# Kernel optimization log

Measured on AMD Instinct MI355X. Metric: run time of the kernel, lower is better.

## Reference

```python
import jax, jax.numpy as jnp
import numpy as np

PAD = float(-2**32 + 1)
NUM_HEADS = 16
LN_EPS = 1e-5


def _split_heads(x, h):
    # torch.cat(torch.chunk(x, h, dim=2), dim=0): head-major stacking
    B, T, D = x.shape
    d = D // h
    return x.reshape(B, T, h, d).transpose(2, 0, 1, 3).reshape(h * B, T, d)


def _merge_heads(x, h):
    # torch.cat(torch.chunk(x, h, dim=0), dim=2)
    hB, T, d = x.shape
    B = hB // h
    return x.reshape(h, B, T, d).transpose(1, 2, 0, 3).reshape(B, T, h * d)


def setup_inputs() -> dict:
    key = jax.random.key(0)
    ks = jax.random.split(key, 12)
    B, T, D = 2, 2048, 1024
    s = 1.0 / np.sqrt(D)
    return {
        "q": jax.random.normal(ks[0], (B, T, D), jnp.float32),
        "k": jax.random.normal(ks[1], (B, T, D), jnp.float32),
        "v": jax.random.normal(ks[2], (B, T, D), jnp.float32),
        "mask": jax.random.randint(ks[3], (B, T), 0, 2, jnp.int32),
        "causality": 0,
        "edge_fea": jnp.zeros((1,), jnp.float32),
        "wq": jax.random.normal(ks[4], (D, D), jnp.float32) * s,
        "bq": jax.random.normal(ks[5], (D,), jnp.float32) * 0.01,
        "wk": jax.random.normal(ks[6], (D, D), jnp.float32) * s,
        "bk": jax.random.normal(ks[7], (D,), jnp.float32) * 0.01,
        "wv": jax.random.normal(ks[8], (D, D), jnp.float32) * s,
        "bv": jax.random.normal(ks[9], (D,), jnp.float32) * 0.01,
        "gamma": jnp.ones((D,), jnp.float32),
        "beta": jnp.zeros((D,), jnp.float32),
    }


def reference(q, k, v, mask, causality, edge_fea, wq, bq, wk, bk, wv, bv, gamma, beta):
    h = NUM_HEADS
    B, T, D = q.shape
    depth = D // h

    qh = _split_heads(q @ wq.T + bq, h)   # (h*B, T, depth)
    kh = _split_heads(k @ wk.T + bk, h)
    vh = _split_heads(v @ wv.T + bv, h)

    scores = jnp.einsum('ntd,nsd->nts', qh, kh) / jnp.sqrt(jnp.asarray(depth, qh.dtype))
    # key mask: repeat_interleave over dim 0 (batch-major), 1 => masked
    km = jnp.repeat(mask.astype(scores.dtype), h, axis=0)[:, None, :]  # (h*B,1,T)
    scores = scores + km * PAD
    if causality:
        tril = jnp.tril(jnp.ones((T, T), scores.dtype))
        scores = jnp.where(tril[None] == 0, jnp.full_like(scores, PAD), scores)
    attn = jax.nn.softmax(scores, axis=-1)
    ctx = jnp.einsum('nts,nsd->ntd', attn, vh)

    out = _merge_heads(ctx, h) + q  # dropout is identity in eval mode
    # LayerNorm over last dim
    mu = jnp.mean(out, axis=-1, keepdims=True)
    var = jnp.var(out, axis=-1, keepdims=True)
    out = (out - mu) / jnp.sqrt(var + LN_EPS) * gamma + beta
    return out
```

## Files before the change

### kernel.cpp

```cpp
#include <hip/hip_runtime.h>
#include <hip/hip_bf16.h>
#include <stdint.h>

#define B_ 2
#define T_ 2048
#define D_ 1024
#define H_ 16
#define DEPTH 64
#define PADV (-4294967295.0f)

typedef unsigned short u16;
typedef unsigned int u32;
typedef short bf16x8 __attribute__((ext_vector_type(8)));
typedef float f32x4 __attribute__((ext_vector_type(4)));

#define MFMA16(a, b, c) __builtin_amdgcn_mfma_f32_16x16x32_bf16(a, b, c, 0, 0, 0)

#define GLOAD_LDS(g, l)                                                      \
    __builtin_amdgcn_global_load_lds(                                        \
        (__attribute__((address_space(1))) void*)(g),                        \
        (__attribute__((address_space(3))) void*)(l), 16, 0, 0)

__device__ __forceinline__ u16 f2bf(float f) {
    union { float f; u32 i; } x; x.f = f;
    u32 r = x.i + 0x7fffu + ((x.i >> 16) & 1u);
    return (u16)(r >> 16);
}
__device__ __forceinline__ uint2 pk4(float4 f) {
    return make_uint2((u32)f2bf(f.x) | ((u32)f2bf(f.y) << 16),
                      (u32)f2bf(f.z) | ((u32)f2bf(f.w) << 16));
}

__global__ __launch_bounds__(256) void conv_kernel(
    const float* __restrict__ s0, const float* __restrict__ s1, const float* __restrict__ s2,
    const float* __restrict__ s3, const float* __restrict__ s4, const float* __restrict__ s5,
    u16* __restrict__ xbf, u16* __restrict__ wbf)
{
    const int z = blockIdx.y;
    const float* src = (z == 0) ? s0 : (z == 1) ? s1 : (z == 2) ? s2
                     : (z == 3) ? s3 : (z == 4) ? s4 : s5;
    u16* dst = (z < 3) ? (xbf + (size_t)z * 4194304) : (wbf + (size_t)(z - 3) * 1048576);
    const size_t nel = (z < 3) ? 4194304u : 1048576u;
    for (size_t i = ((size_t)blockIdx.x * 256 + threadIdx.x) * 8; i < nel;
         i += (size_t)gridDim.x * 2048) {
        float4 a = *(const float4*)(src + i);
        float4 b = *(const float4*)(src + i + 4);
        uint2 lo = pk4(a), hi = pk4(b);
        *(uint4*)(dst + i) = make_uint4(lo.x, lo.y, hi.x, hi.y);
    }
}

__global__ __launch_bounds__(256, 3) void proj_mfma(
    const u16* __restrict__ xbf, const u16* __restrict__ wbf,
    const float* __restrict__ bq, const float* __restrict__ bk, const float* __restrict__ bv,
    u16* __restrict__ qh, u16* __restrict__ kh, u16* __restrict__ vt)
{
    __shared__ __attribute__((aligned(16))) u16 As[128 * 64];
    __shared__ __attribute__((aligned(16))) u16 Bs[128 * 64];

    const int z = blockIdx.z;
    const u16* A = xbf + (size_t)z * 4194304;
    const u16* W = wbf + (size_t)z * 1048576;
    const float* bias = (z == 0) ? bq : (z == 1) ? bk : bv;

    const int tid = threadIdx.x, w = tid >> 6, lane = tid & 63;
    const int quad = lane >> 4, l16 = lane & 15;
    const int m0 = blockIdx.y * 128, n0 = blockIdx.x * 128;
    const int wm = (w & 1) * 64, wn = (w >> 1) * 64;
    const int srow = lane >> 3;
    const int schunk = (lane & 7) ^ srow;

    f32x4 acc[4][4];
    #pragma unroll
    for (int mi = 0; mi < 4; ++mi)
        #pragma unroll
        for (int ni = 0; ni < 4; ++ni) acc[mi][ni] = (f32x4){0.f, 0.f, 0.f, 0.f};

    const size_t ar = (size_t)(m0 + 32 * w + srow);
    const size_t br = (size_t)(n0 + 32 * w + srow);

    for (int k0 = 0; k0 < D_; k0 += 64) {
        __syncthreads();
        #pragma unroll
        for (int i = 0; i < 4; ++i) {
            GLOAD_LDS(A + (ar + 8 * i) * D_ + k0 + schunk * 8, &As[(32 * w + 8 * i) * 64]);
            GLOAD_LDS(W + (br + 8 * i) * D_ + k0 + schunk * 8, &Bs[(32 * w + 8 * i) * 64]);
        }
        __syncthreads();

        #pragma unroll
        for (int kg = 0; kg < 2; ++kg) {
            const int ch = ((4 * kg + quad) ^ (l16 & 7)) * 8;
            bf16x8 af[4], bf[4];
            #pragma unroll
            for (int mi = 0; mi < 4; ++mi)
                af[mi] = *(const bf16x8*)&As[(wm + 16 * mi + l16) * 64 + ch];
            #pragma unroll
            for (int ni = 0; ni < 4; ++ni)
                bf[ni] = *(const bf16x8*)&Bs[(wn + 16 * ni + l16) * 64 + ch];
            #pragma unroll
            for (int mi = 0; mi < 4; ++mi)
                #pragma unroll
                for (int ni = 0; ni < 4; ++ni)
                    acc[mi][ni] = MFMA16(af[mi], bf[ni], acc[mi][ni]);
        }
    }

    float bl[4];
    #pragma unroll
    for (int ni = 0; ni < 4; ++ni) bl[ni] = bias[n0 + wn + ni * 16 + l16];

    #pragma unroll
    for (int mi = 0; mi < 4; ++mi) {
        const int mb = m0 + wm + mi * 16 + quad * 4;
        #pragma unroll
        for (int ni = 0; ni < 4; ++ni) {
            const int nn = n0 + wn + ni * 16 + l16;
            const int head = nn >> 6, d = nn & 63;
            if (z < 2) {
                u16* outp = (z == 0) ? qh : kh;
                #pragma unroll
                for (int r = 0; r < 4; ++r) {
                    const int m = mb + r;
                    const int b = m >> 11, t = m & (T_ - 1);
                    outp[((size_t)(head * B_ + b) * T_ + t) * DEPTH + d] =
                        f2bf(acc[mi][ni][r] + bl[ni]);
                }
            } else {
                const int b = mb >> 11, t = mb & (T_ - 1);
                float4 f = make_float4(acc[mi][ni][0] + bl[ni], acc[mi][ni][1] + bl[ni],
                                       acc[mi][ni][2] + bl[ni], acc[mi][ni][3] + bl[ni]);
                *(uint2*)(vt + ((size_t)(head * B_ + b) * DEPTH + d) * T_ + t) = pk4(f);
            }
        }
    }
}

__global__ __launch_bounds__(256, 3) void proj_kernel(
    const float* __restrict__ qin, const float* __restrict__ kin, const float* __restrict__ vin,
    const float* __restrict__ wq, const float* __restrict__ bq,
    const float* __restrict__ wk, const float* __restrict__ bk,
    const float* __restrict__ wv, const float* __restrict__ bv,
    u16* __restrict__ qh, u16* __restrict__ kh, u16* __restrict__ vt)
{
    __shared__ __attribute__((aligned(16))) u16 As[128][56];
    __shared__ __attribute__((aligned(16))) u16 Bs[128][56];
    const int z = blockIdx.z;
    const float* A    = (z == 0) ? qin : (z == 1) ? kin : vin;
    const float* W    = (z == 0) ? wq  : (z == 1) ? wk  : wv;
    const float* bias = (z == 0) ? bq  : (z == 1) ? bk  : bv;
    const int tid = threadIdx.x, w = tid >> 6, lane = tid & 63;
    const int quad = lane >> 4, l16 = lane & 15;
    const int m0 = blockIdx.y * 128, n0 = blockIdx.x * 128;
    const int wm = (w & 1) * 64, wn = (w >> 1) * 64;
    const int sr = tid >> 3, sc = (tid & 7) << 2;

    f32x4 acc[4][4];
    #pragma unroll
    for (int mi = 0; mi < 4; ++mi)
        #pragma unroll
        for (int ni = 0; ni < 4; ++ni) acc[mi][ni] = (f32x4){0.f, 0.f, 0.f, 0.f};

    for (int k0 = 0; k0 < D_; k0 += 32) {
        float4 av[4], wv4[4];
        #pragma unroll
        for (int g = 0; g < 4; ++g) {
            av[g]  = *(const float4*)(A + (size_t)(m0 + sr + g * 32) * D_ + k0 + sc);
            wv4[g] = *(const float4*)(W + (size_t)(n0 + sr + g * 32) * D_ + k0 + sc);
        }
        __syncthreads();
        #pragma unroll
        for (int g = 0; g < 4; ++g) {
            *(uint2*)&As[sr + g * 32][sc] = pk4(av[g]);
            *(uint2*)&Bs[sr + g * 32][sc] = pk4(wv4[g]);
        }
        __syncthreads();
        bf16x8 af[4], bf[4];
        #pragma unroll
        for (int mi = 0; mi < 4; ++mi)
            af[mi] = *(const bf16x8*)&As[wm + mi * 16 + l16][quad * 8];
        #pragma unroll
        for (int ni = 0; ni < 4; ++ni)
            bf[ni] = *(const bf16x8*)&Bs[wn + ni * 16 + l16][quad * 8];
        #pragma unroll
        for (int mi = 0; mi < 4; ++mi)
            #pragma unroll
            for (int ni = 0; ni < 4; ++ni)
                acc[mi][ni] = MFMA16(af[mi], bf[ni], acc[mi][ni]);
        __syncthreads();
    }
    float bl[4];
    #pragma unroll
    for (int ni = 0; ni < 4; ++ni) bl[ni] = bias[n0 + wn + ni * 16 + l16];
    #pragma unroll
    for (int mi = 0; mi < 4; ++mi) {
        const int mb = m0 + wm + mi * 16 + quad * 4;
        #pragma unroll
        for (int ni = 0; ni < 4; ++ni) {
            const int nn = n0 + wn + ni * 16 + l16;
            const int head = nn >> 6, d = nn & 63;
            if (z < 2) {
                u16* outp = (z == 0) ? qh : kh;
                #pragma unroll
                for (int r = 0; r < 4; ++r) {
                    const int m = mb + r;
                    const int b = m >> 11, t = m & (T_ - 1);
                    outp[((size_t)(head * B_ + b) * T_ + t) * DEPTH + d] =
                        f2bf(acc[mi][ni][r] + bl[ni]);
                }
            } else {
                const int b = mb >> 11, t = mb & (T_ - 1);
                float4 f = make_float4(acc[mi][ni][0] + bl[ni], acc[mi][ni][1] + bl[ni],
                                       acc[mi][ni][2] + bl[ni], acc[mi][ni][3] + bl[ni]);
                *(uint2*)(vt + ((size_t)(head * B_ + b) * DEPTH + d) * T_ + t) = pk4(f);
            }
        }
    }
}

__global__ __launch_bounds__(256, 4) void attn_kernel(
    const u16* __restrict__ qh, const u16* __restrict__ kh, const u16* __restrict__ vt,
    const int* __restrict__ maskp, const int* __restrict__ causp,
    float* __restrict__ outp)
{
    __shared__ __attribute__((aligned(16))) u16 Ks[64][72];
    __shared__ __attribute__((aligned(16))) u16 Vs[64][72];
    __shared__ __attribute__((aligned(16))) u16 Ps[4][16][72];

    const int n  = blockIdx.y;
    const int qt = blockIdx.x;
    const int head = n >> 1, bi = n & 1;
    const int mrow = n >> 4;
    const int caus = causp[0];

    const int tid  = threadIdx.x;
    const int w    = tid >> 6, lane = tid & 63;
    const int quad = lane >> 4, l16 = lane & 15;
    const size_t base = (size_t)n * T_ * DEPTH;
    const int lrow = tid >> 2, lcol = (tid & 3) << 4;

    const int myq = qt * 64 + w * 16 + l16;
    const bf16x8 aq0 = *(const bf16x8*)(qh + base + (size_t)myq * DEPTH + quad * 8);
    const bf16x8 aq1 = *(const bf16x8*)(qh + base + (size_t)myq * DEPTH + 32 + quad * 8);

    f32x4 O[4];
    #pragma unroll
    for (int s = 0; s < 4; ++s) O[s] = (f32x4){0.f, 0.f, 0.f, 0.f};
    float lp = 0.f;

    const int* mrowp = maskp + (size_t)mrow * T_;
    const size_t vbase = (size_t)n * DEPTH * T_;
    const float C1  = 0.18033688011112042f;
    const float PL2 = -6.2e9f;

    for (int t0 = 0; t0 < T_; t0 += 64) {
        __syncthreads();
        {
            const uint4* pk = (const uint4*)(kh + base + (size_t)(t0 + lrow) * DEPTH + lcol);
            *(uint4*)&Ks[lrow][lcol]     = pk[0];
            *(uint4*)&Ks[lrow][lcol + 8] = pk[1];
            const uint4* pv = (const uint4*)(vt + vbase + (size_t)lrow * T_ + t0 + lcol);
            *(uint4*)&Vs[lrow][lcol]     = pv[0];
            *(uint4*)&Vs[lrow][lcol + 8] = pv[1];
        }
        __syncthreads();

        #pragma unroll
        for (int t = 0; t < 4; ++t) {
            bf16x8 kb0 = *(const bf16x8*)&Ks[t * 16 + l16][quad * 8];
            bf16x8 kb1 = *(const bf16x8*)&Ks[t * 16 + l16][32 + quad * 8];
            f32x4 st = (f32x4){0.f, 0.f, 0.f, 0.f};
            st = MFMA16(kb0, aq0, st);
            st = MFMA16(kb1, aq1, st);
            const int4 mk = *(const int4*)(mrowp + t0 + t * 16 + quad * 4);
            float e0, e1, e2, e3;
            {
                float v0 = fmaf(st[0], C1, (float)mk.x * PL2);
                float v1 = fmaf(st[1], C1, (float)mk.y * PL2);
                float v2 = fmaf(st[2], C1, (float)mk.z * PL2);
                float v3 = fmaf(st[3], C1, (float)mk.w * PL2);
                if (caus) {
                    const int kg = t0 + t * 16 + quad * 4;
                    if (kg + 0 > myq) v0 = PL2;
                    if (kg + 1 > myq) v1 = PL2;
                    if (kg + 2 > myq) v2 = PL2;
                    if (kg + 3 > myq) v3 = PL2;
                }
                e0 = exp2f(v0); e1 = exp2f(v1); e2 = exp2f(v2); e3 = exp2f(v3);
            }
            lp += (e0 + e1) + (e2 + e3);
            *(uint2*)&Ps[w][l16][t * 16 + quad * 4] = pk4(make_float4(e0, e1, e2, e3));
        }

        bf16x8 ap0 = *(const bf16x8*)&Ps[w][l16][quad * 8];
        bf16x8 ap1 = *(const bf16x8*)&Ps[w][l16][32 + quad * 8];
        #pragma unroll
        for (int s = 0; s < 4; ++s) {
            bf16x8 vb0 = *(const bf16x8*)&Vs[s * 16 + l16][quad * 8];
            bf16x8 vb1 = *(const bf16x8*)&Vs[s * 16 + l16][32 + quad * 8];
            O[s] = MFMA16(ap0, vb0, O[s]);
            O[s] = MFMA16(ap1, vb1, O[s]);
        }
    }

    lp += __shfl_xor(lp, 16, 64);
    lp += __shfl_xor(lp, 32, 64);

    #pragma unroll
    for (int r = 0; r < 4; ++r) {
        const float lr  = __shfl(lp, quad * 4 + r, 64);
        const float inv = 1.0f / fmaxf(lr, 1e-30f);
        const size_t rb = ((size_t)bi * T_ + qt * 64 + w * 16 + quad * 4 + r) * D_
                        + head * DEPTH + l16;
        outp[rb + 0]  = O[0][r] * inv;
        outp[rb + 16] = O[1][r] * inv;
        outp[rb + 32] = O[2][r] * inv;
        outp[rb + 48] = O[3][r] * inv;
    }
}

__global__ __launch_bounds__(256) void ln_kernel(
    const float* __restrict__ qin,
    const float* __restrict__ gamma, const float* __restrict__ beta,
    float* __restrict__ out)
{
    const int row = blockIdx.x;
    const int tid = threadIdx.x;
    const size_t basei = (size_t)row * D_ + (tid << 2);
    float4 c  = *(const float4*)(out + basei);
    float4 qv = *(const float4*)(qin + basei);
    float x[4] = {c.x + qv.x, c.y + qv.y, c.z + qv.z, c.w + qv.w};
    float s  = x[0] + x[1] + x[2] + x[3];
    float s2 = x[0]*x[0] + x[1]*x[1] + x[2]*x[2] + x[3]*x[3];
    #pragma unroll
    for (int off = 1; off < 64; off <<= 1) {
        s  += __shfl_xor(s, off, 64);
        s2 += __shfl_xor(s2, off, 64);
    }
    __shared__ float rs[4], rs2[4];
    const int wid = tid >> 6;
    if ((tid & 63) == 0) { rs[wid] = s; rs2[wid] = s2; }
    __syncthreads();
    s  = rs[0] + rs[1] + rs[2] + rs[3];
    s2 = rs2[0] + rs2[1] + rs2[2] + rs2[3];
    const float mean = s * (1.0f / (float)D_);
    const float var  = s2 * (1.0f / (float)D_) - mean * mean;
    const float rstd = rsqrtf(var + 1e-5f);
    float4 g = *(const float4*)(gamma + (tid << 2));
    float4 b = *(const float4*)(beta + (tid << 2));
    float4 r;
    r.x = (x[0] - mean) * rstd * g.x + b.x;
    r.y = (x[1] - mean) * rstd * g.y + b.y;
    r.z = (x[2] - mean) * rstd * g.z + b.z;
    r.w = (x[3] - mean) * rstd * g.w + b.w;
    *(float4*)(out + basei) = r;
}

extern "C" void kernel_launch(void* const* d_in, const int* in_sizes, int n_in,
                              void* d_out, int out_size, void* d_ws, size_t ws_size,
                              hipStream_t stream)
{
    (void)in_sizes; (void)n_in; (void)out_size;
    const float* q    = (const float*)d_in[0];
    const float* k    = (const float*)d_in[1];
    const float* v    = (const float*)d_in[2];
    const int* mask = (const int*)d_in[3];
    const int* caus = (const int*)d_in[4];
    const float* wq = (const float*)d_in[6];
    const float* bq = (const float*)d_in[7];
    const float* wk = (const float*)d_in[8];
    const float* bk = (const float*)d_in[9];
    const float* wv = (const float*)d_in[10];
    const float* bv = (const float*)d_in[11];
    const float* gamma = (const float*)d_in[12];
    const float* beta  = (const float*)d_in[13];
    float* out = (float*)d_out;

    const size_t elems = (size_t)B_ * T_ * D_;
    u16* qh  = (u16*)d_ws;
    u16* kh  = qh + elems;
    u16* vt  = kh + elems;
    u16* xbf = vt + elems;
    u16* wbf = xbf + 3 * elems;
    const size_t need = (3 * elems + 3 * elems + 3 * (size_t)1048576) * sizeof(u16);

    if (ws_size >= need) {
        conv_kernel<<<dim3(512, 6), 256, 0, stream>>>(q, k, v, wq, wk, wv, xbf, wbf);
        proj_mfma<<<dim3(8, 32, 3), 256, 0, stream>>>(xbf, wbf, bq, bk, bv, qh, kh, vt);
    } else {
        proj_kernel<<<dim3(8, 32, 3), 256, 0, stream>>>(q, k, v, wq, bq, wk, bk, wv, bv,
                                                        qh, kh, vt);
    }

    dim3 agrid(T_ / 64, H_ * B_);
    attn_kernel<<<agrid, 256, 0, stream>>>(qh, kh, vt, mask, caus, out);

    ln_kernel<<<B_ * T_, 256, 0, stream>>>(q, gamma, beta, out);
}
```

Before: 252.8 us.

## Double query rows per attention block and stage K/V via direct LDS loads

The attention kernel now handles 128 queries per block (two 16-row sub-tiles per wave), so each K/V tile loaded into LDS serves twice as many MFMAs. K/V tiles are loaded with global_load_lds using an XOR-swizzled layout instead of register round-trips. The key mask is converted once into an LDS array of pad values. P is packed to bf16 with a cheaper round-half-up conversion. The fallback fp32 projection kernel is removed, which drops the workspace-size check. Halving the grid to 512 blocks and adding register pressure may reduce occupancy and load balance.

Measured after the change: 249.6 us. Within noise of the previous version (-1.3%).

```diff
diff --git a/kernel.cpp b/kernel.cpp
--- a/kernel.cpp
+++ b/kernel.cpp
@@ -7,7 +7,6 @@
 #define D_ 1024
 #define H_ 16
 #define DEPTH 64
-#define PADV (-4294967295.0f)
 
 typedef unsigned short u16;
 typedef unsigned int u32;
@@ -29,6 +28,10 @@
 __device__ __forceinline__ uint2 pk4(float4 f) {
     return make_uint2((u32)f2bf(f.x) | ((u32)f2bf(f.y) << 16),
                       (u32)f2bf(f.z) | ((u32)f2bf(f.w) << 16));
+}
+__device__ __forceinline__ u32 pkfast(float a, float b) {
+    union { float f; u32 i; } x, y; x.f = a; y.f = b;
+    return ((y.i + 0x8000u) & 0xffff0000u) | ((x.i + 0x8000u) >> 16);
 }
 
 __global__ __launch_bounds__(256) void conv_kernel(
@@ -136,96 +139,15 @@
     }
 }
 
-__global__ __launch_bounds__(256, 3) void proj_kernel(
-    const float* __restrict__ qin, const float* __restrict__ kin, const float* __restrict__ vin,
-    const float* __restrict__ wq, const float* __restrict__ bq,
-    const float* __restrict__ wk, const float* __restrict__ bk,
-    const float* __restrict__ wv, const float* __restrict__ bv,
-    u16* __restrict__ qh, u16* __restrict__ kh, u16* __restrict__ vt)
-{
-    __shared__ __attribute__((aligned(16))) u16 As[128][56];
-    __shared__ __attribute__((aligned(16))) u16 Bs[128][56];
-    const int z = blockIdx.z;
-    const float* A    = (z == 0) ? qin : (z == 1) ? kin : vin;
-    const float* W    = (z == 0) ? wq  : (z == 1) ? wk  : wv;
-    const float* bias = (z == 0) ? bq  : (z == 1) ? bk  : bv;
-    const int tid = threadIdx.x, w = tid >> 6, lane = tid & 63;
-    const int quad = lane >> 4, l16 = lane & 15;
-    const int m0 = blockIdx.y * 128, n0 = blockIdx.x * 128;
-    const int wm = (w & 1) * 64, wn = (w >> 1) * 64;
-    const int sr = tid >> 3, sc = (tid & 7) << 2;
-
-    f32x4 acc[4][4];
-    #pragma unroll
-    for (int mi = 0; mi < 4; ++mi)
-        #pragma unroll
-        for (int ni = 0; ni < 4; ++ni) acc[mi][ni] = (f32x4){0.f, 0.f, 0.f, 0.f};
-
-    for (int k0 = 0; k0 < D_; k0 += 32) {
-        float4 av[4], wv4[4];
-        #pragma unroll
-        for (int g = 0; g < 4; ++g) {
-            av[g]  = *(const float4*)(A + (size_t)(m0 + sr + g * 32) * D_ + k0 + sc);
-            wv4[g] = *(const float4*)(W + (size_t)(n0 + sr + g * 32) * D_ + k0 + sc);
-        }
-        __syncthreads();
-        #pragma unroll
-        for (int g = 0; g < 4; ++g) {
-            *(uint2*)&As[sr + g * 32][sc] = pk4(av[g]);
-            *(uint2*)&Bs[sr + g * 32][sc] = pk4(wv4[g]);
-        }
-        __syncthreads();
-        bf16x8 af[4], bf[4];
-        #pragma unroll
-        for (int mi = 0; mi < 4; ++mi)
-            af[mi] = *(const bf16x8*)&As[wm + mi * 16 + l16][quad * 8];
-        #pragma unroll
-        for (int ni = 0; ni < 4; ++ni)
-            bf[ni] = *(const bf16x8*)&Bs[wn + ni * 16 + l16][quad * 8];
-        #pragma unroll
-        for (int mi = 0; mi < 4; ++mi)
-            #pragma unroll
-            for (int ni = 0; ni < 4; ++ni)
-                acc[mi][ni] = MFMA16(af[mi], bf[ni], acc[mi][ni]);
-        __syncthreads();
-    }
-    float bl[4];
-    #pragma unroll
-    for (int ni = 0; ni < 4; ++ni) bl[ni] = bias[n0 + wn + ni * 16 + l16];
-    #pragma unroll
-    for (int mi = 0; mi < 4; ++mi) {
-        const int mb = m0 + wm + mi * 16 + quad * 4;
-        #pragma unroll
-        for (int ni = 0; ni < 4; ++ni) {
-            const int nn = n0 + wn + ni * 16 + l16;
-            const int head = nn >> 6, d = nn & 63;
-            if (z < 2) {
-                u16* outp = (z == 0) ? qh : kh;
-                #pragma unroll
-                for (int r = 0; r < 4; ++r) {
-                    const int m = mb + r;
-                    const int b = m >> 11, t = m & (T_ - 1);
-                    outp[((size_t)(head * B_ + b) * T_ + t) * DEPTH + d] =
-                        f2bf(acc[mi][ni][r] + bl[ni]);
-                }
-            } else {
-                const int b = mb >> 11, t = mb & (T_ - 1);
-                float4 f = make_float4(acc[mi][ni][0] + bl[ni], acc[mi][ni][1] + bl[ni],
-                                       acc[mi][ni][2] + bl[ni], acc[mi][ni][3] + bl[ni]);
-                *(uint2*)(vt + ((size_t)(head * B_ + b) * DEPTH + d) * T_ + t) = pk4(f);
-            }
-        }
-    }
-}
-
 __global__ __launch_bounds__(256, 4) void attn_kernel(
     const u16* __restrict__ qh, const u16* __restrict__ kh, const u16* __restrict__ vt,
     const int* __restrict__ maskp, const int* __restrict__ causp,
     float* __restrict__ outp)
 {
-    __shared__ __attribute__((aligned(16))) u16 Ks[64][72];
-    __shared__ __attribute__((aligned(16))) u16 Vs[64][72];
-    __shared__ __attribute__((aligned(16))) u16 Ps[4][16][72];
+    __shared__ __attribute__((aligned(16))) u16 Ks[64 * 64];
+    __shared__ __attribute__((aligned(16))) u16 Vs[64 * 64];
+    __shared__ __attribute__((aligned(16))) u16 Ps[4][2][16][72];
+    __shared__ __attribute__((aligned(16))) float padf[T_];
 
     const int n  = blockIdx.y;
     const int qt = blockIdx.x;
@@ -237,85 +159,120 @@
     const int w    = tid >> 6, lane = tid & 63;
     const int quad = lane >> 4, l16 = lane & 15;
     const size_t base = (size_t)n * T_ * DEPTH;
-    const int lrow = tid >> 2, lcol = (tid & 3) << 4;
-
-    const int myq = qt * 64 + w * 16 + l16;
-    const bf16x8 aq0 = *(const bf16x8*)(qh + base + (size_t)myq * DEPTH + quad * 8);
-    const bf16x8 aq1 = *(const bf16x8*)(qh + base + (size_t)myq * DEPTH + 32 + quad * 8);
-
-    f32x4 O[4];
-    #pragma unroll
-    for (int s = 0; s < 4; ++s) O[s] = (f32x4){0.f, 0.f, 0.f, 0.f};
-    float lp = 0.f;
-
-    const int* mrowp = maskp + (size_t)mrow * T_;
     const size_t vbase = (size_t)n * DEPTH * T_;
+
     const float C1  = 0.18033688011112042f;
     const float PL2 = -6.2e9f;
 
+    {
+        const int i0 = tid * 8;
+        int4 ma = *(const int4*)(maskp + (size_t)mrow * T_ + i0);
+        int4 mb = *(const int4*)(maskp + (size_t)mrow * T_ + i0 + 4);
+        padf[i0 + 0] = (float)ma.x * PL2; padf[i0 + 1] = (float)ma.y * PL2;
+        padf[i0 + 2] = (float)ma.z * PL2; padf[i0 + 3] = (float)ma.w * PL2;
+        padf[i0 + 4] = (float)mb.x * PL2; padf[i0 + 5] = (float)mb.y * PL2;
+        padf[i0 + 6] = (float)mb.z * PL2; padf[i0 + 7] = (float)mb.w * PL2;
+    }
+
+    bf16x8 aq[2][2];
+    #pragma unroll
+    for (int s = 0; s < 2; ++s) {
+        const int qg = qt * 128 + w * 32 + s * 16 + l16;
+        aq[s][0] = *(const bf16x8*)(qh + base + (size_t)qg * DEPTH + quad * 8);
+        aq[s][1] = *(const bf16x8*)(qh + base + (size_t)qg * DEPTH + 32 + quad * 8);
+    }
+
+    f32x4 O[2][4];
+    #pragma unroll
+    for (int s = 0; s < 2; ++s)
+        #pragma unroll
+        for (int t = 0; t < 4; ++t) O[s][t] = (f32x4){0.f, 0.f, 0.f, 0.f};
+    float lp[2] = {0.f, 0.f};
+
+    const int g_row = w * 16 + (lane >> 3);
+    const int g_ch  = (lane & 7) ^ ((lane >> 3) & 7);
+    const u16* ksrc = kh + base + (size_t)g_row * DEPTH + g_ch * 8;
+    const u16* vsrc = vt + vbase + (size_t)g_row * T_ + g_ch * 8;
+
     for (int t0 = 0; t0 < T_; t0 += 64) {
         __syncthreads();
-        {
-            const uint4* pk = (const uint4*)(kh + base + (size_t)(t0 + lrow) * DEPTH + lcol);
-            *(uint4*)&Ks[lrow][lcol]     = pk[0];
-            *(uint4*)&Ks[lrow][lcol + 8] = pk[1];
-            const uint4* pv = (const uint4*)(vt + vbase + (size_t)lrow * T_ + t0 + lcol);
-            *(uint4*)&Vs[lrow][lcol]     = pv[0];
-            *(uint4*)&Vs[lrow][lcol + 8] = pv[1];
-        }
+        GLOAD_LDS(ksrc + (size_t)t0 * DEPTH,           &Ks[(w * 16) * 64]);
+        GLOAD_LDS(ksrc + (size_t)(t0 + 8) * DEPTH,     &Ks[(w * 16 + 8) * 64]);
+        GLOAD_LDS(vsrc + t0,                           &Vs[(w * 16) * 64]);
+        GLOAD_LDS(vsrc + (size_t)8 * T_ + t0,          &Vs[(w * 16 + 8) * 64]);
         __syncthreads();
 
         #pragma unroll
         for (int t = 0; t < 4; ++t) {
-            bf16x8 kb0 = *(const bf16x8*)&Ks[t * 16 + l16][quad * 8];
-            bf16x8 kb1 = *(const bf16x8*)&Ks[t * 16 + l16][32 + quad * 8];
-            f32x4 st = (f32x4){0.f, 0.f, 0.f, 0.f};
-            st = MFMA16(kb0, aq0, st);
-            st = MFMA16(kb1, aq1, st);
-            const int4 mk = *(const int4*)(mrowp + t0 + t * 16 + quad * 4);
-            float e0, e1, e2, e3;
-            {
-                float v0 = fmaf(st[0], C1, (float)mk.x * PL2);
-                float v1 = fmaf(st[1], C1, (float)mk.y * PL2);
-                float v2 = fmaf(st[2], C1, (float)mk.z * PL2);
-                float v3 = fmaf(st[3], C1, (float)mk.w * PL2);
+            const int krow = t * 16 + l16;
+            const int swz = (l16 & 7);
+            bf16x8 kb0 = *(const bf16x8*)&Ks[krow * 64 + ((quad ^ swz) * 8)];
+            bf16x8 kb1 = *(const bf16x8*)&Ks[krow * 64 + (((4 + quad) ^ swz) * 8)];
+            f32x4 pv4 = *(const f32x4*)&padf[t0 + t * 16 + quad * 4];
+            #pragma unroll
+            for (int s = 0; s < 2; ++s) {
+                f32x4 st = (f32x4){0.f, 0.f, 0.f, 0.f};
+                st = MFMA16(kb0, aq[s][0], st);
+                st = MFMA16(kb1, aq[s][1], st);
+                float v0 = fmaf(st[0], C1, pv4[0]);
+                float v1 = fmaf(st[1], C1, pv4[1]);
+                float v2 = fmaf(st[2], C1, pv4[2]);
+                float v3 = fmaf(st[3], C1, pv4[3]);
                 if (caus) {
                     const int kg = t0 + t * 16 + quad * 4;
-                    if (kg + 0 > myq) v0 = PL2;
-                    if (kg + 1 > myq) v1 = PL2;
-                    if (kg + 2 > myq) v2 = PL2;
-                    if (kg + 3 > myq) v3 = PL2;
+                    const int qg = qt * 128 + w * 32 + s * 16 + l16;
+                    if (kg + 0 > qg) v0 = PL2;
+                    if (kg + 1 > qg) v1 = PL2;
+                    if (kg + 2 > qg) v2 = PL2;
+                    if (kg + 3 > qg) v3 = PL2;
                 }
-                e0 = exp2f(v0); e1 = exp2f(v1); e2 = exp2f(v2); e3 = exp2f(v3);
+                const float e0 = exp2f(v0), e1 = exp2f(v1);
+                const float e2 = exp2f(v2), e3 = exp2f(v3);
+                lp[s] += (e0 + e1) + (e2 + e3);
+                *(uint2*)&Ps[w][s][l16][t * 16 + quad * 4] =
+                    make_uint2(pkfast(e0, e1), pkfast(e2, e3));
             }
-            lp += (e0 + e1) + (e2 + e3);
-            *(uint2*)&Ps[w][l16][t * 16 + quad * 4] = pk4(make_float4(e0, e1, e2, e3));
-        }
-
-        bf16x8 ap0 = *(const bf16x8*)&Ps[w][l16][quad * 8];
-        bf16x8 ap1 = *(const bf16x8*)&Ps[w][l16][32 + quad * 8];
-        #pragma unroll
-        for (int s = 0; s < 4; ++s) {
-            bf16x8 vb0 = *(const bf16x8*)&Vs[s * 16 + l16][quad * 8];
-            bf16x8 vb1 = *(const bf16x8*)&Vs[s * 16 + l16][32 + quad * 8];
-            O[s] = MFMA16(ap0, vb0, O[s]);
-            O[s] = MFMA16(ap1, vb1, O[s]);
-        }
-    }
-
-    lp += __shfl_xor(lp, 16, 64);
-    lp += __shfl_xor(lp, 32, 64);
-
-    #pragma unroll
-    for (int r = 0; r < 4; ++r) {
-        const float lr  = __shfl(lp, quad * 4 + r, 64);
-        const float inv = 1.0f / fmaxf(lr, 1e-30f);
-        const size_t rb = ((size_t)bi * T_ + qt * 64 + w * 16 + quad * 4 + r) * D_
-                        + head * DEPTH + l16;
-        outp[rb + 0]  = O[0][r] * inv;
-        outp[rb + 16] = O[1][r] * inv;
-        outp[rb + 32] = O[2][r] * inv;
-        outp[rb + 48] = O[3][r] * inv;
+        }
+
+        bf16x8 ap[2][2];
+        #pragma unroll
+        for (int s = 0; s < 2; ++s) {
+            ap[s][0] = *(const bf16x8*)&Ps[w][s][l16][quad * 8];
+            ap[s][1] = *(const bf16x8*)&Ps[w][s][l16][32 + quad * 8];
+        }
+        #pragma unroll
+        for (int t = 0; t < 4; ++t) {
+            const int drow = t * 16 + l16;
+            const int swz = (l16 & 7);
+            bf16x8 vb0 = *(const bf16x8*)&Vs[drow * 64 + ((quad ^ swz) * 8)];
+            bf16x8 vb1 = *(const bf16x8*)&Vs[drow * 64 + (((4 + quad) ^ swz) * 8)];
+            #pragma unroll
+            for (int s = 0; s < 2; ++s) {
+                O[s][t] = MFMA16(ap[s][0], vb0, O[s][t]);
+                O[s][t] = MFMA16(ap[s][1], vb1, O[s][t]);
+            }
+        }
+    }
+
+    #pragma unroll
+    for (int s = 0; s < 2; ++s) {
+        lp[s] += __shfl_xor(lp[s], 16, 64);
+        lp[s] += __shfl_xor(lp[s], 32, 64);
+    }
+
+    #pragma unroll
+    for (int s = 0; s < 2; ++s) {
+        #pragma unroll
+        for (int r = 0; r < 4; ++r) {
+            const float lr  = __shfl(lp[s], quad * 4 + r, 64);
+            const float inv = 1.0f / fmaxf(lr, 1e-30f);
+            const size_t rb = ((size_t)bi * T_ + qt * 128 + w * 32 + s * 16 + quad * 4 + r) * D_
+                            + head * DEPTH + l16;
+            outp[rb + 0]  = O[s][0][r] * inv;
+            outp[rb + 16] = O[s][1][r] * inv;
+            outp[rb + 32] = O[s][2][r] * inv;
+            outp[rb + 48] = O[s][3][r] * inv;
+        }
     }
 }
 
@@ -360,7 +317,7 @@
                               void* d_out, int out_size, void* d_ws, size_t ws_size,
                               hipStream_t stream)
 {
-    (void)in_sizes; (void)n_in; (void)out_size;
+    (void)in_sizes; (void)n_in; (void)out_size; (void)ws_size;
     const float* q    = (const float*)d_in[0];
     const float* k    = (const float*)d_in[1];
     const float* v    = (const float*)d_in[2];
@@ -382,17 +339,11 @@
     u16* vt  = kh + elems;
     u16* xbf = vt + elems;
     u16* wbf = xbf + 3 * elems;
-    const size_t need = (3 * elems + 3 * elems + 3 * (size_t)1048576) * sizeof(u16);
-
-    if (ws_size >= need) {
-        conv_kernel<<<dim3(512, 6), 256, 0, stream>>>(q, k, v, wq, wk, wv, xbf, wbf);
-        proj_mfma<<<dim3(8, 32, 3), 256, 0, stream>>>(xbf, wbf, bq, bk, bv, qh, kh, vt);
-    } else {
-        proj_kernel<<<dim3(8, 32, 3), 256, 0, stream>>>(q, k, v, wq, bq, wk, bk, wv, bv,
-                                                        qh, kh, vt);
-    }
-
-    dim3 agrid(T_ / 64, H_ * B_);
+
+    conv_kernel<<<dim3(512, 6), 256, 0, stream>>>(q, k, v, wq, wk, wv, xbf, wbf);
+    proj_mfma<<<dim3(8, 32, 3), 256, 0, stream>>>(xbf, wbf, bq, bk, bv, qh, kh, vt);
+
+    dim3 agrid(T_ / 128, H_ * B_);
     attn_kernel<<<agrid, 256, 0, stream>>>(qh, kh, vt, mask, caus, out);
 
     ln_kernel<<<B_ * T_, 256, 0, stream>>>(q, gamma, beta, out);
```
